# Performance work log

Hardware: AMD Instinct MI355X
Metric: run time of the kernel (lower is better)

Reference implementation:

```python
import jax, jax.numpy as jnp
import numpy as np

B, C, L = 8, 256, 1024
N_HEAD = 8
GROUPS = 32
EPS = 1e-5


def group_norm(x, gamma, beta):
    # x: [B, C, L]
    b, c, l = x.shape
    xg = x.reshape(b, GROUPS, (c // GROUPS) * l)
    mu = xg.mean(-1, keepdims=True)
    var = xg.var(-1, keepdims=True)
    xg = (xg - mu) / jnp.sqrt(var + EPS)
    x = xg.reshape(b, c, l)
    return x * gamma[None, :, None] + beta[None, :, None]


def conv1d(x, w, b=None, groups=1):
    # x: [B,C,L], w: [O, I/groups, K]
    k = w.shape[-1]
    pad = (k - 1) // 2
    y = jax.lax.conv_general_dilated(
        x, w, window_strides=(1,), padding=[(pad, pad)],
        dimension_numbers=('NCH', 'OIH', 'NCH'),
        feature_group_count=groups)
    if b is not None:
        y = y + b[None, :, None]
    return y


def setup_inputs() -> dict:
    key = jax.random.key(0)
    ks = jax.random.split(key, 8)
    x = jax.random.normal(ks[0], (B, C, L), dtype=jnp.float32)
    gamma = jnp.ones((C,), jnp.float32)
    beta = jnp.zeros((C,), jnp.float32)
    # depthwise conv: torch weight [C,1,3], kaiming_normal fan_in=1*3
    dw_w = jax.random.normal(ks[1], (C, 1, 3), jnp.float32) * np.sqrt(2.0 / 3.0)
    # qkv 1x1 conv: [3C, C, 1], kaiming fan_in=C
    qkv_w = jax.random.normal(ks[2], (3 * C, C, 1), jnp.float32) * np.sqrt(2.0 / C)
    qkv_b = jnp.zeros((3 * C,), jnp.float32)
    out_w = jax.random.normal(ks[3], (C, C, 1), jnp.float32) * np.sqrt(2.0 / C)
    out_b = jnp.zeros((C,), jnp.float32)
    return {"x": x, "gamma": gamma, "beta": beta, "dw_w": dw_w,
            "qkv_w": qkv_w, "qkv_b": qkv_b, "out_w": out_w, "out_b": out_b}


def reference(x, gamma, beta, dw_w, qkv_w, qkv_b, out_w, out_b):
    b, c, l = x.shape
    head_dim = c // N_HEAD
    h = group_norm(x, gamma, beta)
    h = conv1d(h, dw_w, groups=c)                 # depthwise k=3
    qkv = conv1d(h, qkv_w, qkv_b)                 # [B, 3C, L]
    qkv = qkv.reshape(b, N_HEAD, head_dim * 3, l)
    q, k, v = jnp.split(qkv, 3, axis=2)           # each [B, H, D, L]
    attn = jnp.einsum('bhdl,bhdL->bhlL', q, k) / jnp.sqrt(jnp.float32(c))
    attn = jax.nn.softmax(attn, axis=-1)
    o = jnp.einsum('bhlL,bhdL->bhdl', attn, v).reshape(b, c, l)
    o = conv1d(o, out_w, out_b)
    return o + x
```

## Files before the change

### kernel.cpp

```cpp
#include <hip/hip_runtime.h>
#include <hip/hip_bf16.h>

#define B_ 8
#define C_ 256
#define L_ 1024
#define NH_ 8
#define EPS_ 1e-5f

typedef __attribute__((ext_vector_type(8))) short bf16x8;
typedef __attribute__((ext_vector_type(4))) float f32x4;

static __device__ inline ushort f2bf(float f) {
  union { __hip_bfloat16 b; ushort u; } c;
  c.b = __float2bfloat16(f);
  return c.u;
}

__global__ __launch_bounds__(256) void gnw_kernel(
    const float* __restrict__ x, const float* __restrict__ gamma,
    const float* __restrict__ beta, const float* __restrict__ dw,
    const float4* __restrict__ qw, const float4* __restrict__ ow,
    uint2* __restrict__ wq, uint2* __restrict__ wo_,
    ushort* __restrict__ ht) {
  __shared__ float hn[8 * L_];
  __shared__ float ws0[4], ws1[4];
  int t = threadIdx.x;
  if (blockIdx.x < 256) {
    int id = blockIdx.x * 256 + t;
    float4 v;
    uint2* dst;
    if (id < 49152) { v = qw[id]; dst = wq + id; }
    else { v = ow[id - 49152]; dst = wo_ + (id - 49152); }
    union { ushort s[4]; uint2 u; } p;
    p.s[0] = f2bf(v.x); p.s[1] = f2bf(v.y); p.s[2] = f2bf(v.z); p.s[3] = f2bf(v.w);
    *dst = p.u;
    return;
  }
  int blk = blockIdx.x - 256;
  int b = blk >> 5, g = blk & 31;
  const size_t base = ((size_t)(b * C_ + g * 8)) * L_;

  float s = 0.f, ss = 0.f;
  float vals[32];
#pragma unroll
  for (int i = 0; i < 32; ++i) {
    int e = t + 256 * i;
    float v = x[base + e];
    vals[i] = v;
    s += v; ss += v * v;
  }
#pragma unroll
  for (int off = 32; off >= 1; off >>= 1) {
    s  += __shfl_xor(s, off);
    ss += __shfl_xor(ss, off);
  }
  int wave = t >> 6;
  if ((t & 63) == 0) { ws0[wave] = s; ws1[wave] = ss; }
  __syncthreads();
  s  = ws0[0] + ws0[1] + ws0[2] + ws0[3];
  ss = ws1[0] + ws1[1] + ws1[2] + ws1[3];
  float mean = s * (1.f / 8192.f);
  float var = ss * (1.f / 8192.f) - mean * mean;
  float rstd = rsqrtf(var + EPS_);

#pragma unroll
  for (int i = 0; i < 32; ++i) {
    int e = t + 256 * i;
    int c = g * 8 + (e >> 10);
    float sc = gamma[c] * rstd;
    hn[e] = (vals[i] - mean) * sc + beta[c];
  }
  __syncthreads();
  float r[32];
#pragma unroll
  for (int i = 0; i < 32; ++i) {
    int e = t + 256 * i;
    int l = e & 1023;
    int c = g * 8 + (i >> 2);
    float w0 = dw[c * 3 + 0], w1 = dw[c * 3 + 1], w2 = dw[c * 3 + 2];
    float a = (l > 0) ? hn[e - 1] : 0.f;
    float m = hn[e];
    float z = (l < 1023) ? hn[e + 1] : 0.f;
    r[i] = w0 * a + w1 * m + w2 * z;
  }
#pragma unroll
  for (int li = 0; li < 4; ++li) {
    int l = t + 256 * li;
    union { ushort s8[8]; uint4 u; } pk;
#pragma unroll
    for (int cl = 0; cl < 8; ++cl) pk.s8[cl] = f2bf(r[4 * cl + li]);
    *(uint4*)(ht + ((size_t)(b * L_ + l)) * 256 + g * 8) = pk.u;
  }
}

__global__ __launch_bounds__(256) void qkv_fused_kernel(
    const ushort* __restrict__ Xt, const ushort* __restrict__ Wb,
    const float* __restrict__ bias, ushort* __restrict__ qt,
    ushort* __restrict__ kt, ushort* __restrict__ vb) {
  int bx = blockIdx.x, head = blockIdx.y, b = blockIdx.z;
  int bh = b * 8 + head;
  int t = threadIdx.x;
  int w = t >> 6, l = t & 63;
  int g = l >> 4, ln = l & 15;
  int wl = w >> 1, wo = w & 1;
  int lbase = bx * 128 + wl * 64;

  const ushort* xp = Xt + ((size_t)b * L_ + lbase) * 256;
  const ushort* wp = Wb + (size_t)(head * 96 + wo * 48) * 256;

  f32x4 acc[4][3];
#pragma unroll
  for (int ml = 0; ml < 4; ++ml)
#pragma unroll
    for (int nn = 0; nn < 3; ++nn) acc[ml][nn] = (f32x4){0.f, 0.f, 0.f, 0.f};

  for (int c0 = 0; c0 < 256; c0 += 32) {
    bf16x8 af[4], bf[3];
#pragma unroll
    for (int ml = 0; ml < 4; ++ml)
      af[ml] = *(const bf16x8*)(xp + (size_t)(16 * ml + ln) * 256 + c0 + 8 * g);
#pragma unroll
    for (int nn = 0; nn < 3; ++nn)
      bf[nn] = *(const bf16x8*)(wp + (size_t)(16 * nn + ln) * 256 + c0 + 8 * g);
#pragma unroll
    for (int ml = 0; ml < 4; ++ml)
#pragma unroll
      for (int nn = 0; nn < 3; ++nn)
        acc[ml][nn] = __builtin_amdgcn_mfma_f32_16x16x32_bf16(af[ml], bf[nn], acc[ml][nn], 0, 0, 0);
  }

#pragma unroll
  for (int nn = 0; nn < 3; ++nn) {
    float bs = bias[head * 96 + wo * 48 + 16 * nn + ln];
#pragma unroll
    for (int ml = 0; ml < 4; ++ml)
#pragma unroll
      for (int r = 0; r < 4; ++r) acc[ml][nn][r] += bs;
  }

  __shared__ ushort tr[5120];
  const float QSC = 0.0625f * 1.44269504f;

  for (int rk = 0; rk < 2; ++rk) {
    float sc = rk ? 1.f : QSC;
    __syncthreads();
#pragma unroll
    for (int nn = 0; nn < 3; ++nn) {
      int ocl0 = wo * 48 + 16 * nn;
      if (ocl0 >= rk * 32 && ocl0 < rk * 32 + 32) {
        int d = ocl0 - rk * 32 + ln;
#pragma unroll
        for (int ml = 0; ml < 4; ++ml) {
          int lrow = wl * 64 + 16 * ml + 4 * g;
#pragma unroll
          for (int r = 0; r < 4; ++r)
            tr[(lrow + r) * 40 + d] = f2bf(acc[ml][nn][r] * sc);
        }
      }
    }
    __syncthreads();
    {
      int row = t >> 1, half = t & 1;
      uint4 v0 = *(const uint4*)&tr[row * 40 + half * 16];
      uint4 v1 = *(const uint4*)&tr[row * 40 + half * 16 + 8];
      ushort* dst = (rk ? kt : qt) +
                    ((size_t)bh * L_ + bx * 128 + row) * 32 + half * 16;
      *(uint4*)dst = v0;
      *(uint4*)(dst + 8) = v1;
    }
  }

  __syncthreads();
  if (wo == 1) {
#pragma unroll
    for (int nn = 1; nn < 3; ++nn) {
      int d = 16 * (nn - 1) + ln;
#pragma unroll
      for (int ml = 0; ml < 4; ++ml) {
        int lc = wl * 64 + 16 * ml + 4 * g;
        union { ushort s[4]; uint2 u; } pk;
#pragma unroll
        for (int r = 0; r < 4; ++r) pk.s[r] = f2bf(acc[ml][nn][r]);
        *(uint2*)&tr[d * 136 + lc] = pk.u;
      }
    }
  }
  __syncthreads();
  {
    int d = t >> 3, s0 = t & 7;
    ushort* vdst = vb + ((size_t)bh * 32 + d) * L_ + bx * 128;
#pragma unroll
    for (int c = 0; c < 2; ++c) {
      int ch = s0 + 8 * c;
      int jj = ch >> 2, gg = ch & 3;
      uint2 lo = *(const uint2*)&tr[d * 136 + 32 * jj + 4 * gg];
      uint2 hi = *(const uint2*)&tr[d * 136 + 32 * jj + 16 + 4 * gg];
      *(uint4*)(vdst + 32 * jj + 8 * gg) = make_uint4(lo.x, lo.y, hi.x, hi.y);
    }
  }
}

template <int OCT>
__global__ __launch_bounds__(256) void pconv_mfma_kernel(
    const ushort* __restrict__ Xt, const ushort* __restrict__ Wb,
    const float* __restrict__ bias, const float* __restrict__ resid,
    float* __restrict__ out, int OC) {
  constexpr int NN = OCT / 16;
  int b = blockIdx.z;
  int t = threadIdx.x;
  int w = t >> 6, l = t & 63;
  int g = l >> 4, ln = l & 15;
  int wl = w >> 1, wo = w & 1;
  int lbase = blockIdx.x * 128 + wl * 64;
  int ocbase = blockIdx.y * (2 * OCT) + wo * OCT;

  const ushort* xp = Xt + ((size_t)b * L_ + lbase) * 256;
  const ushort* wp = Wb + (size_t)ocbase * 256;

  f32x4 acc[4][NN];
#pragma unroll
  for (int ml = 0; ml < 4; ++ml)
#pragma unroll
    for (int nn = 0; nn < NN; ++nn) acc[ml][nn] = (f32x4){0.f, 0.f, 0.f, 0.f};

  for (int c0 = 0; c0 < 256; c0 += 32) {
    bf16x8 af[4], bf[NN];
#pragma unroll
    for (int ml = 0; ml < 4; ++ml)
      af[ml] = *(const bf16x8*)(xp + (size_t)(16 * ml + ln) * 256 + c0 + 8 * g);
#pragma unroll
    for (int nn = 0; nn < NN; ++nn)
      bf[nn] = *(const bf16x8*)(wp + (size_t)(16 * nn + ln) * 256 + c0 + 8 * g);
#pragma unroll
    for (int ml = 0; ml < 4; ++ml)
#pragma unroll
      for (int nn = 0; nn < NN; ++nn)
        acc[ml][nn] = __builtin_amdgcn_mfma_f32_16x16x32_bf16(af[ml], bf[nn], acc[ml][nn], 0, 0, 0);
  }

#pragma unroll
  for (int nn = 0; nn < NN; ++nn) {
    int oc = ocbase + 16 * nn + ln;
    float bs = bias[oc];
#pragma unroll
    for (int ml = 0; ml < 4; ++ml) {
      int lr = lbase + 16 * ml + 4 * g;
      size_t ob = ((size_t)b * OC + oc) * L_ + lr;
      float4 rd = *(const float4*)(resid + ob);
      float4 st = make_float4(acc[ml][nn][0] + bs + rd.x, acc[ml][nn][1] + bs + rd.y,
                              acc[ml][nn][2] + bs + rd.z, acc[ml][nn][3] + bs + rd.w);
      *(float4*)(out + ob) = st;
    }
  }
}

__global__ __launch_bounds__(256) void attn_mfma_kernel(
    const ushort* __restrict__ qt, const ushort* __restrict__ kt,
    const ushort* __restrict__ vb, ushort* __restrict__ ot) {
  const int id = blockIdx.x;
  const int bh = ((id & 7) << 3) | (id >> 6);
  const int qtile = (id >> 3) & 7;
  const int b = bh >> 3, hh = bh & 7;
  const int t = threadIdx.x;
  const int w = t >> 6, l = t & 63;
  const int g = l >> 4, ln = l & 15;
  const int q0b = qtile * 128;
  const int q0 = q0b + w * 32;

  __shared__ ushort Kl[2][128 * 40];
  __shared__ ushort Vl[2][32 * 136];
  __shared__ __align__(16) ushort otile[128][40];

  const ushort* qbase = qt + (size_t)bh * (L_ * 32);
  const ushort* kbase = kt + (size_t)bh * (L_ * 32);
  const ushort* vbase = vb + (size_t)bh * (32 * L_);

  const int krow = t >> 1, khalf = t & 1;
  const ushort* kg = kbase + krow * 32 + khalf * 16;
  const int kwo = krow * 40 + khalf * 16;
  const int vrow = t >> 3, vc = (t & 7) * 16;
  const ushort* vg = vbase + (size_t)vrow * L_ + vc;
  const int vwo = vrow * 136 + vc;

  const f32x4 z4 = {0.f, 0.f, 0.f, 0.f};
  bf16x8 bq[2];
  bq[0] = *(const bf16x8*)(qbase + (size_t)(q0 + ln) * 32 + g * 8);
  bq[1] = *(const bf16x8*)(qbase + (size_t)(q0 + 16 + ln) * 32 + g * 8);

  union { ushort s[8]; bf16x8 v; } onesu;
#pragma unroll
  for (int i = 0; i < 8; ++i) onesu.s[i] = 0x3F80;
  const bf16x8 ones = onesu.v;

  f32x4 oacc[2][2];
  oacc[0][0] = z4; oacc[0][1] = z4; oacc[1][0] = z4; oacc[1][1] = z4;
  f32x4 oaccS[2] = {z4, z4};

  uint4 ka0, ka1, va0, va1;
  ka0 = *(const uint4*)kg;       ka1 = *(const uint4*)(kg + 8);
  va0 = *(const uint4*)vg;       va1 = *(const uint4*)(vg + 8);
  __builtin_amdgcn_sched_barrier(0);
  *(uint4*)&Kl[0][kwo] = ka0;    *(uint4*)&Kl[0][kwo + 8] = ka1;
  *(uint4*)&Vl[0][vwo] = va0;    *(uint4*)&Vl[0][vwo + 8] = va1;
  asm volatile("s_waitcnt lgkmcnt(0)" ::: "memory");
  __builtin_amdgcn_s_barrier();
  __builtin_amdgcn_sched_barrier(0);

  for (int tt = 0; tt < 8; ++tt) {
    const int cur = tt & 1;
    if (tt < 7) {
      ka0 = *(const uint4*)(kg + (tt + 1) * 4096);
      ka1 = *(const uint4*)(kg + (tt + 1) * 4096 + 8);
      va0 = *(const uint4*)(vg + (tt + 1) * 128);
      va1 = *(const uint4*)(vg + (tt + 1) * 128 + 8);
    }
    __builtin_amdgcn_sched_barrier(0);

    const ushort* Kc = &Kl[cur][0];
    const ushort* Vc = &Vl[cur][0];

    f32x4 sacc[8][2];
#pragma unroll
    for (int mk = 0; mk < 8; ++mk) {
      bf16x8 ak = *(const bf16x8*)(Kc + (16 * mk + ln) * 40 + g * 8);
      sacc[mk][0] = __builtin_amdgcn_mfma_f32_16x16x32_bf16(ak, bq[0], z4, 0, 0, 0);
      sacc[mk][1] = __builtin_amdgcn_mfma_f32_16x16x32_bf16(ak, bq[1], z4, 0, 0, 0);
    }

    uint upk[2][8][2];
#pragma unroll
    for (int nq = 0; nq < 2; ++nq) {
#pragma unroll
      for (int mk = 0; mk < 8; ++mk) {
        float e0 = __builtin_amdgcn_exp2f(sacc[mk][nq][0]);
        float e1 = __builtin_amdgcn_exp2f(sacc[mk][nq][1]);
        float e2 = __builtin_amdgcn_exp2f(sacc[mk][nq][2]);
        float e3 = __builtin_amdgcn_exp2f(sacc[mk][nq][3]);
        union { ushort s[4]; uint u[2]; } pk;
        pk.s[0] = f2bf(e0); pk.s[1] = f2bf(e1);
        pk.s[2] = f2bf(e2); pk.s[3] = f2bf(e3);
        upk[nq][mk][0] = pk.u[0]; upk[nq][mk][1] = pk.u[1];
      }
    }

#pragma unroll
    for (int ks = 0; ks < 4; ++ks) {
      union { uint u[4]; bf16x8 v; } pb0, pb1;
      pb0.u[0] = upk[0][2 * ks][0]; pb0.u[1] = upk[0][2 * ks][1];
      pb0.u[2] = upk[0][2 * ks + 1][0]; pb0.u[3] = upk[0][2 * ks + 1][1];
      pb1.u[0] = upk[1][2 * ks][0]; pb1.u[1] = upk[1][2 * ks][1];
      pb1.u[2] = upk[1][2 * ks + 1][0]; pb1.u[3] = upk[1][2 * ks + 1][1];
      oaccS[0] = __builtin_amdgcn_mfma_f32_16x16x32_bf16(ones, pb0.v, oaccS[0], 0, 0, 0);
      oaccS[1] = __builtin_amdgcn_mfma_f32_16x16x32_bf16(ones, pb1.v, oaccS[1], 0, 0, 0);
#pragma unroll
      for (int md = 0; md < 2; ++md) {
        bf16x8 av = *(const bf16x8*)(Vc + (16 * md + ln) * 136 + 32 * ks + 8 * g);
        oacc[md][0] = __builtin_amdgcn_mfma_f32_16x16x32_bf16(av, pb0.v, oacc[md][0], 0, 0, 0);
        oacc[md][1] = __builtin_amdgcn_mfma_f32_16x16x32_bf16(av, pb1.v, oacc[md][1], 0, 0, 0);
      }
    }

    __builtin_amdgcn_sched_barrier(0);
    if (tt < 7) {
      const int nxt = cur ^ 1;
      *(uint4*)&Kl[nxt][kwo] = ka0;  *(uint4*)&Kl[nxt][kwo + 8] = ka1;
      *(uint4*)&Vl[nxt][vwo] = va0;  *(uint4*)&Vl[nxt][vwo + 8] = va1;
      asm volatile("s_waitcnt lgkmcnt(0)" ::: "memory");
      __builtin_amdgcn_s_barrier();
      __builtin_amdgcn_sched_barrier(0);
    }
  }

  float rl0 = 1.f / oaccS[0][0];
  float rl1 = 1.f / oaccS[1][0];
#pragma unroll
  for (int md = 0; md < 2; ++md) {
    ushort4 p0, p1;
    p0.x = f2bf(oacc[md][0][0] * rl0); p0.y = f2bf(oacc[md][0][1] * rl0);
    p0.z = f2bf(oacc[md][0][2] * rl0); p0.w = f2bf(oacc[md][0][3] * rl0);
    p1.x = f2bf(oacc[md][1][0] * rl1); p1.y = f2bf(oacc[md][1][1] * rl1);
    p1.z = f2bf(oacc[md][1][2] * rl1); p1.w = f2bf(oacc[md][1][3] * rl1);
    *(ushort4*)&otile[w * 32 + ln][16 * md + 4 * g] = p0;
    *(ushort4*)&otile[w * 32 + 16 + ln][16 * md + 4 * g] = p1;
  }
  __syncthreads();
  {
    int row = t >> 1, half = t & 1;
    uint4 v0 = *(const uint4*)&otile[row][half * 16];
    uint4 v1 = *(const uint4*)&otile[row][half * 16 + 8];
    ushort* dstp = ot + ((size_t)(b * L_ + q0b + row)) * 256 + hh * 32 + half * 16;
    *(uint4*)dstp = v0;
    *(uint4*)(dstp + 8) = v1;
  }
}

extern "C" void kernel_launch(void* const* d_in, const int* in_sizes, int n_in,
                              void* d_out, int out_size, void* d_ws, size_t ws_size,
                              hipStream_t stream) {
  const float* x      = (const float*)d_in[0];
  const float* gamma  = (const float*)d_in[1];
  const float* beta   = (const float*)d_in[2];
  const float* dw     = (const float*)d_in[3];
  const float* qkv_w  = (const float*)d_in[4];
  const float* qkv_b  = (const float*)d_in[5];
  const float* out_w  = (const float*)d_in[6];
  const float* out_b  = (const float*)d_in[7];
  float* out = (float*)d_out;

  char* ws = (char*)d_ws;
  ushort* ht   = (ushort*)(ws);
  ushort* qtb  = (ushort*)(ws + (16u << 20));
  ushort* ktb  = (ushort*)(ws + (20u << 20));
  ushort* vbb  = (ushort*)(ws + (24u << 20));
  ushort* otb  = (ushort*)(ws);
  ushort* wq   = (ushort*)(ws + (28u << 20));
  ushort* wo   = (ushort*)(ws + (28u << 20) + (512u << 10));

  gnw_kernel<<<512, 256, 0, stream>>>(x, gamma, beta, dw,
                                      (const float4*)qkv_w, (const float4*)out_w,
                                      (uint2*)wq, (uint2*)wo, ht);
  qkv_fused_kernel<<<dim3(8, 8, B_), 256, 0, stream>>>(ht, wq, qkv_b, qtb, ktb, vbb);
  attn_mfma_kernel<<<512, 256, 0, stream>>>(qtb, ktb, vbb, otb);
  pconv_mfma_kernel<32><<<dim3(8, 4, B_), 256, 0, stream>>>(
      otb, wo, out_b, x, out, 256);
}
```

Baseline: 62.88 us.

## Block intermediate activation layouts by channel group and restage output conv stores

The normalized activations are now stored channel-blocked ([b][group][L][8]) instead of position-major with 256 channels per row. The attention output is likewise stored per head ([bh][L][32]). Both changes make the A-fragment loads in the qkv and output convolutions read contiguous rows. The output conv now uses 16 output channels per wave on a grid twice as large, and stages results through shared memory so the residual add and stores are fully coalesced float4 rows. Attention shared buffers are merged into one array to reuse the K region for the output tile, which lowers LDS footprint and may raise occupancy. The cost is an extra sync and LDS pass in the output conv and less weight reuse per block.

```diff
diff --git a/kernel.cpp b/kernel.cpp
--- a/kernel.cpp
+++ b/kernel.cpp
@@ -89,7 +89,7 @@
     union { ushort s8[8]; uint4 u; } pk;
 #pragma unroll
     for (int cl = 0; cl < 8; ++cl) pk.s8[cl] = f2bf(r[4 * cl + li]);
-    *(uint4*)(ht + ((size_t)(b * L_ + l)) * 256 + g * 8) = pk.u;
+    *(uint4*)(ht + (((size_t)(b * 32 + g)) * L_ + l) * 8) = pk.u;
   }
 }
 
@@ -105,7 +105,7 @@
   int wl = w >> 1, wo = w & 1;
   int lbase = bx * 128 + wl * 64;
 
-  const ushort* xp = Xt + ((size_t)b * L_ + lbase) * 256;
+  const ushort* xb = Xt + (size_t)b * (32 * L_ * 8);
   const ushort* wp = Wb + (size_t)(head * 96 + wo * 48) * 256;
 
   f32x4 acc[4][3];
@@ -118,7 +118,8 @@
     bf16x8 af[4], bf[3];
 #pragma unroll
     for (int ml = 0; ml < 4; ++ml)
-      af[ml] = *(const bf16x8*)(xp + (size_t)(16 * ml + ln) * 256 + c0 + 8 * g);
+      af[ml] = *(const bf16x8*)(xb +
+          (((size_t)((c0 >> 3) + g)) * L_ + lbase + 16 * ml + ln) * 8);
 #pragma unroll
     for (int nn = 0; nn < 3; ++nn)
       bf[nn] = *(const bf16x8*)(wp + (size_t)(16 * nn + ln) * 256 + c0 + 8 * g);
@@ -200,56 +201,58 @@
   }
 }
 
-template <int OCT>
-__global__ __launch_bounds__(256) void pconv_mfma_kernel(
+__global__ __launch_bounds__(256) void outconv_kernel(
     const ushort* __restrict__ Xt, const ushort* __restrict__ Wb,
     const float* __restrict__ bias, const float* __restrict__ resid,
-    float* __restrict__ out, int OC) {
-  constexpr int NN = OCT / 16;
+    float* __restrict__ out) {
   int b = blockIdx.z;
   int t = threadIdx.x;
   int w = t >> 6, l = t & 63;
   int g = l >> 4, ln = l & 15;
   int wl = w >> 1, wo = w & 1;
   int lbase = blockIdx.x * 128 + wl * 64;
-  int ocbase = blockIdx.y * (2 * OCT) + wo * OCT;
-
-  const ushort* xp = Xt + ((size_t)b * L_ + lbase) * 256;
+  int ocblk = blockIdx.y * 32;
+  int ocbase = ocblk + wo * 16;
+
+  const ushort* xb = Xt + (size_t)b * (8 * L_ * 32);
   const ushort* wp = Wb + (size_t)ocbase * 256;
 
-  f32x4 acc[4][NN];
-#pragma unroll
-  for (int ml = 0; ml < 4; ++ml)
-#pragma unroll
-    for (int nn = 0; nn < NN; ++nn) acc[ml][nn] = (f32x4){0.f, 0.f, 0.f, 0.f};
+  f32x4 acc[4];
+#pragma unroll
+  for (int ml = 0; ml < 4; ++ml) acc[ml] = (f32x4){0.f, 0.f, 0.f, 0.f};
 
   for (int c0 = 0; c0 < 256; c0 += 32) {
-    bf16x8 af[4], bf[NN];
+    bf16x8 af[4];
 #pragma unroll
     for (int ml = 0; ml < 4; ++ml)
-      af[ml] = *(const bf16x8*)(xp + (size_t)(16 * ml + ln) * 256 + c0 + 8 * g);
-#pragma unroll
-    for (int nn = 0; nn < NN; ++nn)
-      bf[nn] = *(const bf16x8*)(wp + (size_t)(16 * nn + ln) * 256 + c0 + 8 * g);
+      af[ml] = *(const bf16x8*)(xb +
+          ((size_t)(c0 >> 5) * L_ + lbase + 16 * ml + ln) * 32 + 8 * g);
+    bf16x8 bf = *(const bf16x8*)(wp + (size_t)ln * 256 + c0 + 8 * g);
 #pragma unroll
     for (int ml = 0; ml < 4; ++ml)
-#pragma unroll
-      for (int nn = 0; nn < NN; ++nn)
-        acc[ml][nn] = __builtin_amdgcn_mfma_f32_16x16x32_bf16(af[ml], bf[nn], acc[ml][nn], 0, 0, 0);
-  }
-
-#pragma unroll
-  for (int nn = 0; nn < NN; ++nn) {
-    int oc = ocbase + 16 * nn + ln;
-    float bs = bias[oc];
-#pragma unroll
-    for (int ml = 0; ml < 4; ++ml) {
-      int lr = lbase + 16 * ml + 4 * g;
-      size_t ob = ((size_t)b * OC + oc) * L_ + lr;
-      float4 rd = *(const float4*)(resid + ob);
-      float4 st = make_float4(acc[ml][nn][0] + bs + rd.x, acc[ml][nn][1] + bs + rd.y,
-                              acc[ml][nn][2] + bs + rd.z, acc[ml][nn][3] + bs + rd.w);
-      *(float4*)(out + ob) = st;
+      acc[ml] = __builtin_amdgcn_mfma_f32_16x16x32_bf16(af[ml], bf, acc[ml], 0, 0, 0);
+  }
+
+  __shared__ float tile[32][132];
+  float bs = bias[ocbase + ln];
+#pragma unroll
+  for (int ml = 0; ml < 4; ++ml) {
+    int ll = wl * 64 + 16 * ml + 4 * g;
+    float4 v = make_float4(acc[ml][0] + bs, acc[ml][1] + bs,
+                           acc[ml][2] + bs, acc[ml][3] + bs);
+    *(float4*)&tile[wo * 16 + ln][ll] = v;
+  }
+  __syncthreads();
+  {
+    int ocl = t >> 3, lq = t & 7;
+    const float* src = &tile[ocl][lq * 16];
+    size_t ob = ((size_t)b * 256 + ocblk + ocl) * L_ + blockIdx.x * 128 + lq * 16;
+#pragma unroll
+    for (int i = 0; i < 4; ++i) {
+      float4 v = *(const float4*)(src + 4 * i);
+      float4 rd = *(const float4*)(resid + ob + 4 * i);
+      v.x += rd.x; v.y += rd.y; v.z += rd.z; v.w += rd.w;
+      *(float4*)(out + ob + 4 * i) = v;
     }
   }
 }
@@ -260,16 +263,13 @@
   const int id = blockIdx.x;
   const int bh = ((id & 7) << 3) | (id >> 6);
   const int qtile = (id >> 3) & 7;
-  const int b = bh >> 3, hh = bh & 7;
   const int t = threadIdx.x;
   const int w = t >> 6, l = t & 63;
   const int g = l >> 4, ln = l & 15;
   const int q0b = qtile * 128;
   const int q0 = q0b + w * 32;
 
-  __shared__ ushort Kl[2][128 * 40];
-  __shared__ ushort Vl[2][32 * 136];
-  __shared__ __align__(16) ushort otile[128][40];
+  __shared__ __align__(16) ushort smem[18944];
 
   const ushort* qbase = qt + (size_t)bh * (L_ * 32);
   const ushort* kbase = kt + (size_t)bh * (L_ * 32);
@@ -300,8 +300,8 @@
   ka0 = *(const uint4*)kg;       ka1 = *(const uint4*)(kg + 8);
   va0 = *(const uint4*)vg;       va1 = *(const uint4*)(vg + 8);
   __builtin_amdgcn_sched_barrier(0);
-  *(uint4*)&Kl[0][kwo] = ka0;    *(uint4*)&Kl[0][kwo + 8] = ka1;
-  *(uint4*)&Vl[0][vwo] = va0;    *(uint4*)&Vl[0][vwo + 8] = va1;
+  *(uint4*)&smem[kwo] = ka0;             *(uint4*)&smem[kwo + 8] = ka1;
+  *(uint4*)&smem[10240 + vwo] = va0;     *(uint4*)&smem[10240 + vwo + 8] = va1;
   asm volatile("s_waitcnt lgkmcnt(0)" ::: "memory");
   __builtin_amdgcn_s_barrier();
   __builtin_amdgcn_sched_barrier(0);
@@ -316,8 +316,8 @@
     }
     __builtin_amdgcn_sched_barrier(0);
 
-    const ushort* Kc = &Kl[cur][0];
-    const ushort* Vc = &Vl[cur][0];
+    const ushort* Kc = &smem[cur * 5120];
+    const ushort* Vc = &smem[10240 + cur * 4352];
 
     f32x4 sacc[8][2];
 #pragma unroll
@@ -363,14 +363,17 @@
     __builtin_amdgcn_sched_barrier(0);
     if (tt < 7) {
       const int nxt = cur ^ 1;
-      *(uint4*)&Kl[nxt][kwo] = ka0;  *(uint4*)&Kl[nxt][kwo + 8] = ka1;
-      *(uint4*)&Vl[nxt][vwo] = va0;  *(uint4*)&Vl[nxt][vwo + 8] = va1;
+      *(uint4*)&smem[nxt * 5120 + kwo] = ka0;
+      *(uint4*)&smem[nxt * 5120 + kwo + 8] = ka1;
+      *(uint4*)&smem[10240 + nxt * 4352 + vwo] = va0;
+      *(uint4*)&smem[10240 + nxt * 4352 + vwo + 8] = va1;
       asm volatile("s_waitcnt lgkmcnt(0)" ::: "memory");
       __builtin_amdgcn_s_barrier();
       __builtin_amdgcn_sched_barrier(0);
     }
   }
 
+  ushort* otile = &smem[0];
   float rl0 = 1.f / oaccS[0][0];
   float rl1 = 1.f / oaccS[1][0];
 #pragma unroll
@@ -380,15 +383,15 @@
     p0.z = f2bf(oacc[md][0][2] * rl0); p0.w = f2bf(oacc[md][0][3] * rl0);
     p1.x = f2bf(oacc[md][1][0] * rl1); p1.y = f2bf(oacc[md][1][1] * rl1);
     p1.z = f2bf(oacc[md][1][2] * rl1); p1.w = f2bf(oacc[md][1][3] * rl1);
-    *(ushort4*)&otile[w * 32 + ln][16 * md + 4 * g] = p0;
-    *(ushort4*)&otile[w * 32 + 16 + ln][16 * md + 4 * g] = p1;
+    *(ushort4*)&otile[(w * 32 + ln) * 40 + 16 * md + 4 * g] = p0;
+    *(ushort4*)&otile[(w * 32 + 16 + ln) * 40 + 16 * md + 4 * g] = p1;
   }
   __syncthreads();
   {
     int row = t >> 1, half = t & 1;
-    uint4 v0 = *(const uint4*)&otile[row][half * 16];
-    uint4 v1 = *(const uint4*)&otile[row][half * 16 + 8];
-    ushort* dstp = ot + ((size_t)(b * L_ + q0b + row)) * 256 + hh * 32 + half * 16;
+    uint4 v0 = *(const uint4*)&otile[row * 40 + half * 16];
+    uint4 v1 = *(const uint4*)&otile[row * 40 + half * 16 + 8];
+    ushort* dstp = ot + ((size_t)bh * L_ + q0b + row) * 32 + half * 16;
     *(uint4*)dstp = v0;
     *(uint4*)(dstp + 8) = v1;
   }
@@ -421,6 +424,5 @@
                                       (uint2*)wq, (uint2*)wo, ht);
   qkv_fused_kernel<<<dim3(8, 8, B_), 256, 0, stream>>>(ht, wq, qkv_b, qtb, ktb, vbb);
   attn_mfma_kernel<<<512, 256, 0, stream>>>(qtb, ktb, vbb, otb);
-  pconv_mfma_kernel<32><<<dim3(8, 4, B_), 256, 0, stream>>>(
-      otb, wo, out_b, x, out, 256);
-}
+  outconv_kernel<<<dim3(8, 8, B_), 256, 0, stream>>>(otb, wo, out_b, x, out);
+}
```

New measurement: 57.91 us. 7.9% less time.
